# Optimization experiments

Hardware: AMD Instinct MI355X
Metric: run time of the kernel (lower is better)

The kernel has to match this reference:

```python
import jax, jax.numpy as jnp
import numpy as np

LAYER_NUMS = 3


def setup_inputs() -> dict:
    key = jax.random.key(0)
    k1, k2 = jax.random.split(key)
    B, D = 8192, 1024
    x = jax.random.normal(k1, (B, D), dtype=jnp.float32)
    W = jax.random.normal(k2, (LAYER_NUMS, D), dtype=jnp.float32)
    b = jnp.zeros((LAYER_NUMS, D), dtype=jnp.float32)
    return {"x": x, "W": W, "b": b}


def reference(x, W, b):
    # DCN cross layer: x_{l+1} = x_0 * (x_l . w_l) + b_l + x_l
    # The torch code materializes the [B,d,d] outer product x_0 x_l^T then
    # contracts with w; algebraically identical to scaling x_0 by the
    # scalar dot product (x_l . w), which we compute directly.
    x0 = x
    x_l = x
    for i in range(LAYER_NUMS):
        scale = jnp.einsum('bd,d->b', x_l, W[i])       # [B]
        x_l = x0 * scale[:, None] + b[i][None, :] + x_l  # [B, d]
    return x_l
```

## Files before the change

### kernel.cpp

```cpp
#include <hip/hip_runtime.h>


#define DDIM 1024
#define RPW 4

typedef float f32x4 __attribute__((ext_vector_type(4)));

__device__ __forceinline__ float dot4(f32x4 a, f32x4 b) {
    return fmaf(a.x, b.x, fmaf(a.y, b.y, fmaf(a.z, b.z, a.w * b.w)));
}

__global__ __launch_bounds__(256) void CrossLayer_kernel(
    const float* __restrict__ x,
    const float* __restrict__ W,
    const float* __restrict__ bias,
    float* __restrict__ out,
    int B)
{
    const int wave = threadIdx.x >> 6;
    const int lane = threadIdx.x & 63;
    const int wid  = blockIdx.x * 4 + wave;
    const int row0 = wid * RPW;
    if (row0 >= B) return;

    const f32x4* w0 = reinterpret_cast<const f32x4*>(W);
    const f32x4* w1 = reinterpret_cast<const f32x4*>(W + DDIM);
    const f32x4* w2 = reinterpret_cast<const f32x4*>(W + 2 * DDIM);
    const f32x4* b0 = reinterpret_cast<const f32x4*>(bias);
    const f32x4* b1 = reinterpret_cast<const f32x4*>(bias + DDIM);
    const f32x4* b2 = reinterpret_cast<const f32x4*>(bias + 2 * DDIM);

    f32x4 x0[RPW][4];
#pragma unroll
    for (int r = 0; r < RPW; ++r) {
        const f32x4* xr = reinterpret_cast<const f32x4*>(x + (size_t)(row0 + r) * DDIM);
#pragma unroll
        for (int c = 0; c < 4; ++c)
            x0[r][c] = xr[c * 64 + lane];
    }

    f32x4 bsum[4];
    float d[RPW][3];
#pragma unroll
    for (int r = 0; r < RPW; ++r) { d[r][0] = d[r][1] = d[r][2] = 0.f; }
    float c1 = 0.f, c2 = 0.f;

#pragma unroll
    for (int c = 0; c < 4; ++c) {
        const int idx = c * 64 + lane;
        f32x4 wv0 = w0[idx], wv1 = w1[idx], wv2 = w2[idx];
        f32x4 bv0 = b0[idx], bv1 = b1[idx], bv2 = b2[idx];
        bsum[c] = bv0 + bv1 + bv2;
        c1 += dot4(bv0, wv1);
        f32x4 b01 = bv0 + bv1;
        c2 += dot4(b01, wv2);
#pragma unroll
        for (int r = 0; r < RPW; ++r) {
            d[r][0] += dot4(x0[r][c], wv0);
            d[r][1] += dot4(x0[r][c], wv1);
            d[r][2] += dot4(x0[r][c], wv2);
        }
    }

#pragma unroll
    for (int off = 32; off > 0; off >>= 1) {
        c1 += __shfl_xor(c1, off, 64);
        c2 += __shfl_xor(c2, off, 64);
#pragma unroll
        for (int r = 0; r < RPW; ++r) {
            d[r][0] += __shfl_xor(d[r][0], off, 64);
            d[r][1] += __shfl_xor(d[r][1], off, 64);
            d[r][2] += __shfl_xor(d[r][2], off, 64);
        }
    }

    float alpha[RPW];
#pragma unroll
    for (int r = 0; r < RPW; ++r) {
        const float t1 = 1.f + d[r][0];
        const float s1 = fmaf(t1, d[r][1], c1);
        const float t2 = t1 + s1;
        const float s2 = fmaf(t2, d[r][2], c2);
        alpha[r] = t2 + s2;
    }

#pragma unroll
    for (int r = 0; r < RPW; ++r) {
        f32x4* orow = reinterpret_cast<f32x4*>(out + (size_t)(row0 + r) * DDIM);
#pragma unroll
        for (int c = 0; c < 4; ++c) {
            f32x4 o;
            o.x = fmaf(x0[r][c].x, alpha[r], bsum[c].x);
            o.y = fmaf(x0[r][c].y, alpha[r], bsum[c].y);
            o.z = fmaf(x0[r][c].z, alpha[r], bsum[c].z);
            o.w = fmaf(x0[r][c].w, alpha[r], bsum[c].w);
            __builtin_nontemporal_store(o, &orow[c * 64 + lane]);
        }
    }
}

extern "C" void kernel_launch(void* const* d_in, const int* in_sizes, int n_in,
                              void* d_out, int out_size, void* d_ws, size_t ws_size,
                              hipStream_t stream) {
    const float* x  = (const float*)d_in[0];
    const float* W  = (const float*)d_in[1];
    const float* b  = (const float*)d_in[2];
    float* out      = (float*)d_out;

    const int B = in_sizes[0] / DDIM;
    const int rows_per_block = 4 * RPW;
    dim3 grid((B + rows_per_block - 1) / rows_per_block), block(256);
    hipLaunchKernelGGL(CrossLayer_kernel, grid, block, 0, stream,
                       x, W, b, out, B);
}
```

Baseline: 14.54 us.

## Double-buffer row loads and process rows sequentially with preloaded weights

Weights and bias sums are now loaded into registers up front. Each wave then processes its rows one at a time, prefetching the next row's x into a second buffer while it computes the current row's dot products, reductions and output. This is meant to shrink live register state and overlap loads with compute. It also swaps the nontemporal stores for regular stores. The trade-off is less load parallelism in flight per wave compared with issuing all row loads at once.

```diff
diff --git a/kernel.cpp b/kernel.cpp
--- a/kernel.cpp
+++ b/kernel.cpp
@@ -23,78 +23,83 @@
     const int row0 = wid * RPW;
     if (row0 >= B) return;
 
-    const f32x4* w0 = reinterpret_cast<const f32x4*>(W);
-    const f32x4* w1 = reinterpret_cast<const f32x4*>(W + DDIM);
-    const f32x4* w2 = reinterpret_cast<const f32x4*>(W + 2 * DDIM);
-    const f32x4* b0 = reinterpret_cast<const f32x4*>(bias);
-    const f32x4* b1 = reinterpret_cast<const f32x4*>(bias + DDIM);
-    const f32x4* b2 = reinterpret_cast<const f32x4*>(bias + 2 * DDIM);
+    const f32x4* w0p = reinterpret_cast<const f32x4*>(W);
+    const f32x4* w1p = reinterpret_cast<const f32x4*>(W + DDIM);
+    const f32x4* w2p = reinterpret_cast<const f32x4*>(W + 2 * DDIM);
+    const f32x4* b0p = reinterpret_cast<const f32x4*>(bias);
+    const f32x4* b1p = reinterpret_cast<const f32x4*>(bias + DDIM);
+    const f32x4* b2p = reinterpret_cast<const f32x4*>(bias + 2 * DDIM);
 
-    f32x4 x0[RPW][4];
-#pragma unroll
-    for (int r = 0; r < RPW; ++r) {
-        const f32x4* xr = reinterpret_cast<const f32x4*>(x + (size_t)(row0 + r) * DDIM);
-#pragma unroll
-        for (int c = 0; c < 4; ++c)
-            x0[r][c] = xr[c * 64 + lane];
-    }
-
-    f32x4 bsum[4];
-    float d[RPW][3];
-#pragma unroll
-    for (int r = 0; r < RPW; ++r) { d[r][0] = d[r][1] = d[r][2] = 0.f; }
+    f32x4 wv[3][4], bsum[4];
     float c1 = 0.f, c2 = 0.f;
-
 #pragma unroll
     for (int c = 0; c < 4; ++c) {
         const int idx = c * 64 + lane;
-        f32x4 wv0 = w0[idx], wv1 = w1[idx], wv2 = w2[idx];
-        f32x4 bv0 = b0[idx], bv1 = b1[idx], bv2 = b2[idx];
+        wv[0][c] = w0p[idx];
+        wv[1][c] = w1p[idx];
+        wv[2][c] = w2p[idx];
+        f32x4 bv0 = b0p[idx], bv1 = b1p[idx], bv2 = b2p[idx];
         bsum[c] = bv0 + bv1 + bv2;
-        c1 += dot4(bv0, wv1);
+        c1 += dot4(bv0, wv[1][c]);
         f32x4 b01 = bv0 + bv1;
-        c2 += dot4(b01, wv2);
-#pragma unroll
-        for (int r = 0; r < RPW; ++r) {
-            d[r][0] += dot4(x0[r][c], wv0);
-            d[r][1] += dot4(x0[r][c], wv1);
-            d[r][2] += dot4(x0[r][c], wv2);
-        }
+        c2 += dot4(b01, wv[2][c]);
     }
 
+    f32x4 xbuf[2][4];
+
+    {
+        const f32x4* xr = reinterpret_cast<const f32x4*>(x + (size_t)row0 * DDIM);
 #pragma unroll
-    for (int off = 32; off > 0; off >>= 1) {
-        c1 += __shfl_xor(c1, off, 64);
-        c2 += __shfl_xor(c2, off, 64);
-#pragma unroll
-        for (int r = 0; r < RPW; ++r) {
-            d[r][0] += __shfl_xor(d[r][0], off, 64);
-            d[r][1] += __shfl_xor(d[r][1], off, 64);
-            d[r][2] += __shfl_xor(d[r][2], off, 64);
-        }
-    }
-
-    float alpha[RPW];
-#pragma unroll
-    for (int r = 0; r < RPW; ++r) {
-        const float t1 = 1.f + d[r][0];
-        const float s1 = fmaf(t1, d[r][1], c1);
-        const float t2 = t1 + s1;
-        const float s2 = fmaf(t2, d[r][2], c2);
-        alpha[r] = t2 + s2;
+        for (int c = 0; c < 4; ++c)
+            xbuf[0][c] = xr[c * 64 + lane];
     }
 
 #pragma unroll
     for (int r = 0; r < RPW; ++r) {
+        const int cur = r & 1, nxt = cur ^ 1;
+
+        if (r + 1 < RPW) {
+            const f32x4* xr = reinterpret_cast<const f32x4*>(
+                x + (size_t)(row0 + r + 1) * DDIM);
+#pragma unroll
+            for (int c = 0; c < 4; ++c)
+                xbuf[nxt][c] = xr[c * 64 + lane];
+        }
+
+        float d0 = 0.f, d1 = 0.f, d2 = 0.f;
+#pragma unroll
+        for (int c = 0; c < 4; ++c) {
+            d0 += dot4(xbuf[cur][c], wv[0][c]);
+            d1 += dot4(xbuf[cur][c], wv[1][c]);
+            d2 += dot4(xbuf[cur][c], wv[2][c]);
+        }
+
+#pragma unroll
+        for (int off = 32; off > 0; off >>= 1) {
+            d0 += __shfl_xor(d0, off, 64);
+            d1 += __shfl_xor(d1, off, 64);
+            d2 += __shfl_xor(d2, off, 64);
+            if (r == 0) {
+                c1 += __shfl_xor(c1, off, 64);
+                c2 += __shfl_xor(c2, off, 64);
+            }
+        }
+
+        const float t1 = 1.f + d0;
+        const float s1 = fmaf(t1, d1, c1);
+        const float t2 = t1 + s1;
+        const float s2 = fmaf(t2, d2, c2);
+        const float alpha = t2 + s2;
+
         f32x4* orow = reinterpret_cast<f32x4*>(out + (size_t)(row0 + r) * DDIM);
 #pragma unroll
         for (int c = 0; c < 4; ++c) {
             f32x4 o;
-            o.x = fmaf(x0[r][c].x, alpha[r], bsum[c].x);
-            o.y = fmaf(x0[r][c].y, alpha[r], bsum[c].y);
-            o.z = fmaf(x0[r][c].z, alpha[r], bsum[c].z);
-            o.w = fmaf(x0[r][c].w, alpha[r], bsum[c].w);
-            __builtin_nontemporal_store(o, &orow[c * 64 + lane]);
+            o.x = fmaf(xbuf[cur][c].x, alpha, bsum[c].x);
+            o.y = fmaf(xbuf[cur][c].y, alpha, bsum[c].y);
+            o.z = fmaf(xbuf[cur][c].z, alpha, bsum[c].z);
+            o.w = fmaf(xbuf[cur][c].w, alpha, bsum[c].w);
+            orow[c * 64 + lane] = o;
         }
     }
 }
```

Result: slower. 16.45 us (+13.1%).
